# Kernel optimization log

Hardware: AMD Instinct MI355X
Metric: run time of the kernel (lower is better)

Reference implementation:

```python
import jax, jax.numpy as jnp
import numpy as np

B, A, S, T, DE, D3 = 8, 32, 16, 750, 25, 58
L, DZ = 4, 512
KL_P = 0.0002


def setup_inputs() -> dict:
    key = jax.random.key(0)
    ks = jax.random.split(key, 6)
    return {
        "gt_emotion": jax.random.normal(ks[0], (B * A, T, DE), jnp.float32),
        "gt_3dmm": jax.random.normal(ks[1], (B * A, T, D3), jnp.float32),
        "pred_emotion": jax.random.normal(ks[2], (B * S, T, DE), jnp.float32),
        "pred_3dmm": jax.random.normal(ks[3], (B * S, T, D3), jnp.float32),
        "dist_mu": jax.random.normal(ks[4], (L, B * S, DZ), jnp.float32),
        "dist_scale": jax.random.uniform(ks[5], (L, B * S, DZ), jnp.float32, 0.5, 1.5),
        "num_appropriate": jnp.full((B,), A, jnp.int32),
        "num_samples": jnp.full((B,), S, jnp.int32),
    }


def reference(gt_emotion, gt_3dmm, pred_emotion, pred_3dmm, dist_mu, dist_scale,
              num_appropriate, num_samples):
    b = num_appropriate.shape[0]
    a = gt_emotion.shape[0] // b      # appropriate reactions per batch element
    s = pred_emotion.shape[0] // b    # predicted samples per batch element
    t, de = gt_emotion.shape[1], gt_emotion.shape[2]
    d3 = gt_3dmm.shape[2]

    ge = gt_emotion.reshape(b, a, t, de)
    g3 = gt_3dmm.reshape(b, a, t, d3)
    pe = pred_emotion.reshape(b, s, t, de)
    p3 = pred_3dmm.reshape(b, s, t, d3)

    # pairwise mean-MSE cost between every pred sample and every appropriate gt
    ce = jnp.mean((pe[:, :, None] - ge[:, None]) ** 2, axis=(3, 4))                    # [b,s,a]
    c1 = jnp.mean((p3[:, :, None, :, :52] - g3[:, None, :, :, :52]) ** 2, axis=(3, 4))
    c2 = jnp.mean((p3[:, :, None, :, 52:] - g3[:, None, :, :, 52:]) ** 2, axis=(3, 4))
    cost = ce + c1 + 10.0 * c2

    idx = jnp.argmin(cost, axis=2)                     # [b,s] best-match index (torch.no_grad)
    bidx = jnp.arange(b)[:, None]
    ge_sel = ge[bidx, idx]                             # [b,s,t,de] gathered gt
    g3_sel = g3[bidx, idx]                             # [b,s,t,d3]

    rec_loss = (jnp.mean((pe - ge_sel) ** 2)
                + jnp.mean((p3[..., :52] - g3_sel[..., :52]) ** 2)
                + 10.0 * jnp.mean((p3[..., 52:] - g3_sel[..., 52:]) ** 2))

    # KL(N(mu, scale) || N(0, 1)), mean per layer then averaged over layers
    kl = -jnp.log(dist_scale) + 0.5 * (dist_scale ** 2 + dist_mu ** 2 - 1.0)
    kld_loss = jnp.mean(kl)

    loss = rec_loss + KL_P * kld_loss
    return (loss, rec_loss, kld_loss)
```

## Files before the change

kernel.cpp:

```cpp
#include <hip/hip_runtime.h>

#define NB 8
#define NA 32
#define NS 16
#define KE 18750
#define K3 43500
#define KH_E 9375
#define KH_3 21750
#define ND3 58
#define NKL 262144

#define SE_SLABS 10
#define SD_SLABS 22
#define SLABS 32
#define CHE 938
#define CHD 989
#define COST_BLOCKS (NB * 8 * SLABS)
#define KL_BLOCKS 64
#define KL_PER_THR (NKL / (KL_BLOCKS * 256))

#define SW_1 0.0050637127f
#define SW_2 0.0471404521f
#define W_E  (1.0f / 18750.0f)

__global__ __launch_bounds__(256, 3) void fused_kernel(
    const float* __restrict__ ge, const float* __restrict__ g3,
    const float* __restrict__ pe, const float* __restrict__ p3,
    const float* __restrict__ mu, const float* __restrict__ sc,
    float* __restrict__ cost, float* __restrict__ klsum)
{
    const int blk = blockIdx.x;
    const int tid = threadIdx.x;
    __shared__ float red[4][64];

    if (blk < KL_BLOCKS) {
        float ks = 0.f;
        #pragma unroll
        for (int it = 0; it < KL_PER_THR; ++it) {
            const int i = blk * (256 * KL_PER_THR) + it * 256 + tid;
            const float m = mu[i], sg = sc[i];
            ks += 0.5f * (sg * sg + m * m - 1.0f) - logf(sg);
        }
        #pragma unroll
        for (int o = 32; o > 0; o >>= 1) ks += __shfl_xor(ks, o);
        const int lane = tid & 63, w = tid >> 6;
        if (lane == 0) red[0][w] = ks;
        __syncthreads();
        if (tid == 0)
            atomicAdd(klsum, red[0][0] + red[0][1] + red[0][2] + red[0][3]);
        return;
    }

    const int cblk = blk - KL_BLOCKS;
    const int b    = cblk >> 8;
    const int rem  = cblk & 255;
    const int pos  = rem >> 5;
    const int slab = rem & 31;
    const int s0   = (pos >> 2) * 8;
    const int a0   = (pos & 3) * 8;

    const bool isE = slab < SE_SLABS;

    float acc[64];
    #pragma unroll
    for (int i = 0; i < 64; ++i) acc[i] = 0.f;

    if (isE) {
        const int base = slab * CHE;
        const int kend = min(base + CHE, KH_E);
        const float2* __restrict__ P = (const float2*)(pe + (size_t)(b * NS + s0) * KE);
        const float2* __restrict__ G = (const float2*)(ge + (size_t)(b * NA + a0) * KE);

        int kk = base + tid;
        float2 p[8], g[8];
        #pragma unroll
        for (int i = 0; i < 8; ++i) p[i] = P[i * KH_E + kk];
        #pragma unroll
        for (int j = 0; j < 8; ++j) g[j] = G[j * KH_E + kk];

        #pragma unroll 1
        while (kk < kend) {
            const int knext = kk + 256;
            const int kload = (knext < kend) ? knext : kk;
            float2 pn[8], gn[8];
            #pragma unroll
            for (int i = 0; i < 8; ++i) pn[i] = P[i * KH_E + kload];
            #pragma unroll
            for (int j = 0; j < 8; ++j) gn[j] = G[j * KH_E + kload];

            #pragma unroll
            for (int i = 0; i < 8; ++i)
                #pragma unroll
                for (int j = 0; j < 8; ++j) {
                    const float d0 = p[i].x - g[j].x;
                    const float d1 = p[i].y - g[j].y;
                    float t = fmaf(d0, d0, acc[i * 8 + j]);
                    acc[i * 8 + j] = fmaf(d1, d1, t);
                }

            #pragma unroll
            for (int i = 0; i < 8; ++i) { p[i] = pn[i]; g[i] = gn[i]; }
            kk = knext;
        }
    } else {
        const int base = (slab - SE_SLABS) * CHD;
        const int kend = min(base + CHD, KH_3);
        const float2* __restrict__ P = (const float2*)(p3 + (size_t)(b * NS + s0) * K3);
        const float2* __restrict__ G = (const float2*)(g3 + (size_t)(b * NA + a0) * K3);

        int kk = base + tid;
        int col = (2 * kk) % ND3;
        float2 p[8], g[8];
        #pragma unroll
        for (int i = 0; i < 8; ++i) p[i] = P[i * KH_3 + kk];
        #pragma unroll
        for (int j = 0; j < 8; ++j) g[j] = G[j * KH_3 + kk];

        #pragma unroll 1
        while (kk < kend) {
            const int knext = kk + 256;
            const int kload = (knext < kend) ? knext : kk;
            float2 pn[8], gn[8];
            #pragma unroll
            for (int i = 0; i < 8; ++i) pn[i] = P[i * KH_3 + kload];
            #pragma unroll
            for (int j = 0; j < 8; ++j) gn[j] = G[j * KH_3 + kload];

            const float sw = (col < 52) ? SW_1 : SW_2;
            col += 48; if (col >= ND3) col -= ND3;

            float2 ps[8], gs[8];
            #pragma unroll
            for (int i = 0; i < 8; ++i) { ps[i].x = p[i].x * sw; ps[i].y = p[i].y * sw; }
            #pragma unroll
            for (int j = 0; j < 8; ++j) { gs[j].x = g[j].x * sw; gs[j].y = g[j].y * sw; }

            #pragma unroll
            for (int i = 0; i < 8; ++i)
                #pragma unroll
                for (int j = 0; j < 8; ++j) {
                    const float d0 = ps[i].x - gs[j].x;
                    const float d1 = ps[i].y - gs[j].y;
                    float t = fmaf(d0, d0, acc[i * 8 + j]);
                    acc[i * 8 + j] = fmaf(d1, d1, t);
                }

            #pragma unroll
            for (int i = 0; i < 8; ++i) { p[i] = pn[i]; g[i] = gn[i]; }
            kk = knext;
        }
    }

    const int lane = tid & 63;
    int n = 64;
    #pragma unroll
    for (int step = 0; step < 6; ++step) {
        const int o = 1 << step;
        const bool hi = (lane & o) != 0;
        const int h = n >> 1;
        #pragma unroll
        for (int m = 0; m < h; ++m) {
            const float send = hi ? acc[m] : acc[m + h];
            const float recv = __shfl_xor(send, o);
            acc[m] = (hi ? acc[m + h] : acc[m]) + recv;
        }
        n = h;
    }

    const int w = tid >> 6;
    red[w][__brev((unsigned)lane) >> 26] = acc[0];
    __syncthreads();
    if (tid < 64) {
        float v = red[0][tid] + red[1][tid] + red[2][tid] + red[3][tid];
        if (isE) v *= W_E;
        const int i = tid >> 3, j = tid & 7;
        atomicAdd(&cost[b * (NS * NA) + (s0 + i) * NA + (a0 + j)], v);
    }
}

__global__ __launch_bounds__(128) void finalize_kernel(
    const float* __restrict__ cost, const float* __restrict__ klsum,
    float* __restrict__ out)
{
    const int t = threadIdx.x;
    const float4* row = (const float4*)(cost + t * NA);
    float mn = 1e30f;
    #pragma unroll
    for (int q = 0; q < 8; ++q) {
        const float4 v = row[q];
        mn = fminf(mn, fminf(fminf(v.x, v.y), fminf(v.z, v.w)));
    }
    #pragma unroll
    for (int o = 32; o > 0; o >>= 1) mn += __shfl_xor(mn, o);
    __shared__ float r2[2];
    if ((t & 63) == 0) r2[t >> 6] = mn;
    __syncthreads();
    if (t == 0) {
        const float rec = (r2[0] + r2[1]) * (1.0f / (NB * NS));
        const float kld = klsum[0] * (1.0f / (float)NKL);
        out[0] = fmaf(0.0002f, kld, rec);
        out[1] = rec;
        out[2] = kld;
    }
}

extern "C" void kernel_launch(void* const* d_in, const int* in_sizes, int n_in,
                              void* d_out, int out_size, void* d_ws, size_t ws_size,
                              hipStream_t stream)
{
    const float* ge = (const float*)d_in[0];
    const float* g3 = (const float*)d_in[1];
    const float* pe = (const float*)d_in[2];
    const float* p3 = (const float*)d_in[3];
    const float* mu = (const float*)d_in[4];
    const float* sc = (const float*)d_in[5];

    float* cost  = (float*)d_ws;
    float* klsum = cost + NB * NS * NA;

    hipMemsetAsync(d_ws, 0, (NB * NS * NA + 1) * sizeof(float), stream);

    fused_kernel<<<COST_BLOCKS + KL_BLOCKS, 256, 0, stream>>>(
        ge, g3, pe, p3, mu, sc, cost, klsum);
    finalize_kernel<<<1, 128, 0, stream>>>(cost, klsum, (float*)d_out);
}
```

Before: 146.0 us.

## Stage pairwise-cost operands through LDS with async global_load_lds double buffering

Replaces direct per-thread float2 register prefetch with asynchronous global-to-LDS loads (global_load_lds, 16 bytes per lane) into a per-wave double buffer, synchronised with explicit vmcnt waits. The reduction dimension is re-split into fixed 256-float2 chunks across fewer, larger slabs (12 per tile instead of 32), and the last partial chunk is masked with a weight. The aim is wider memory transactions, fewer in-flight registers and fewer redundant atomics and blocks. The cost is more LDS per block, occupancy lowered to 2, and reliance on hand-written waitcnt correctness.

```diff
diff --git a/kernel.cpp b/kernel.cpp
--- a/kernel.cpp
+++ b/kernel.cpp
@@ -1,4 +1,5 @@
 #include <hip/hip_runtime.h>
+#include <stdint.h>
 
 #define NB 8
 #define NA 32
@@ -10,11 +11,12 @@
 #define ND3 58
 #define NKL 262144
 
-#define SE_SLABS 10
-#define SD_SLABS 22
-#define SLABS 32
-#define CHE 938
-#define CHD 989
+#define CHUNK_F2 256
+#define NCH_E 37
+#define NCH_D 85
+#define E_SLABS 4
+#define D_SLABS 8
+#define SLABS 12
 #define COST_BLOCKS (NB * 8 * SLABS)
 #define KL_BLOCKS 64
 #define KL_PER_THR (NKL / (KL_BLOCKS * 256))
@@ -23,15 +25,19 @@
 #define SW_2 0.0471404521f
 #define W_E  (1.0f / 18750.0f)
 
-__global__ __launch_bounds__(256, 3) void fused_kernel(
+__global__ __launch_bounds__(256, 2) void fused_kernel(
     const float* __restrict__ ge, const float* __restrict__ g3,
     const float* __restrict__ pe, const float* __restrict__ p3,
     const float* __restrict__ mu, const float* __restrict__ sc,
     float* __restrict__ cost, float* __restrict__ klsum)
 {
+    __shared__ float lds[4][2][16][128];
+    float* red = &lds[0][0][0][0];
+
     const int blk = blockIdx.x;
     const int tid = threadIdx.x;
-    __shared__ float red[4][64];
+    const int w   = tid >> 6;
+    const int l   = tid & 63;
 
     if (blk < KL_BLOCKS) {
         float ks = 0.f;
@@ -43,51 +49,75 @@
         }
         #pragma unroll
         for (int o = 32; o > 0; o >>= 1) ks += __shfl_xor(ks, o);
-        const int lane = tid & 63, w = tid >> 6;
-        if (lane == 0) red[0][w] = ks;
+        if (l == 0) red[w] = ks;
         __syncthreads();
         if (tid == 0)
-            atomicAdd(klsum, red[0][0] + red[0][1] + red[0][2] + red[0][3]);
+            atomicAdd(klsum, red[0] + red[1] + red[2] + red[3]);
         return;
     }
 
     const int cblk = blk - KL_BLOCKS;
-    const int b    = cblk >> 8;
-    const int rem  = cblk & 255;
-    const int pos  = rem >> 5;
-    const int slab = rem & 31;
+    const int b    = cblk / (8 * SLABS);
+    const int rem  = cblk % (8 * SLABS);
+    const int pos  = rem / SLABS;
+    const int slab = rem % SLABS;
     const int s0   = (pos >> 2) * 8;
     const int a0   = (pos & 3) * 8;
 
-    const bool isE = slab < SE_SLABS;
+    const bool isE = slab < E_SLABS;
+    const int  KF  = isE ? KE : K3;
+    const int  KH  = isE ? KH_E : KH_3;
+    int clo, chi;
+    if (isE) { clo = slab * NCH_E / E_SLABS; chi = (slab + 1) * NCH_E / E_SLABS; }
+    else {
+        const int ds = slab - E_SLABS;
+        clo = ds * NCH_D / D_SLABS; chi = (ds + 1) * NCH_D / D_SLABS;
+    }
+
+    const float* __restrict__ Pr = isE ? pe + (size_t)(b * NS + s0) * KE
+                                       : p3 + (size_t)(b * NS + s0) * K3;
+    const float* __restrict__ Gr = isE ? ge + (size_t)(b * NA + a0) * KE
+                                       : g3 + (size_t)(b * NA + a0) * K3;
+
+    float* wb0 = &lds[w][0][0][0];
+    float* wb1 = &lds[w][1][0][0];
 
     float acc[64];
     #pragma unroll
     for (int i = 0; i < 64; ++i) acc[i] = 0.f;
 
+    const int rsel = l >> 5;
+    const int coff = (l & 31) * 2;
+    auto STAGE = [&](int c, float* wb) {
+        int f2 = c * CHUNK_F2 + w * 64 + coff;
+        f2 = (f2 <= KH - 2) ? f2 : (KH - 2);
+        #pragma unroll
+        for (int t = 0; t < 8; ++t) {
+            const float* src = (t < 4)
+                ? Pr + (size_t)(2 * t + rsel) * KF + 2 * f2
+                : Gr + (size_t)(2 * (t - 4) + rsel) * KF + 2 * f2;
+            __builtin_amdgcn_global_load_lds(
+                (const __attribute__((address_space(1))) uint32_t*)src,
+                (__attribute__((address_space(3))) uint32_t*)(wb + t * 256),
+                16, 0, 0);
+        }
+    };
+
+    int col = (2 * (clo * CHUNK_F2 + w * 64 + l)) % ND3;
+
+    STAGE(clo, (clo & 1) ? wb1 : wb0);
+
     if (isE) {
-        const int base = slab * CHE;
-        const int kend = min(base + CHE, KH_E);
-        const float2* __restrict__ P = (const float2*)(pe + (size_t)(b * NS + s0) * KE);
-        const float2* __restrict__ G = (const float2*)(ge + (size_t)(b * NA + a0) * KE);
-
-        int kk = base + tid;
-        float2 p[8], g[8];
-        #pragma unroll
-        for (int i = 0; i < 8; ++i) p[i] = P[i * KH_E + kk];
-        #pragma unroll
-        for (int j = 0; j < 8; ++j) g[j] = G[j * KH_E + kk];
-
         #pragma unroll 1
-        while (kk < kend) {
-            const int knext = kk + 256;
-            const int kload = (knext < kend) ? knext : kk;
-            float2 pn[8], gn[8];
-            #pragma unroll
-            for (int i = 0; i < 8; ++i) pn[i] = P[i * KH_E + kload];
-            #pragma unroll
-            for (int j = 0; j < 8; ++j) gn[j] = G[j * KH_E + kload];
-
+        for (int c = clo; c < chi - 1; ++c) {
+            STAGE(c + 1, ((c + 1) & 1) ? wb1 : wb0);
+            asm volatile("s_waitcnt vmcnt(8)" ::: "memory");
+            const float* wb = (c & 1) ? wb1 : wb0;
+            float2 p[8], g[8];
+            #pragma unroll
+            for (int i = 0; i < 8; ++i) p[i] = *(const float2*)(wb + i * 128 + 2 * l);
+            #pragma unroll
+            for (int j = 0; j < 8; ++j) g[j] = *(const float2*)(wb + (8 + j) * 128 + 2 * l);
             #pragma unroll
             for (int i = 0; i < 8; ++i)
                 #pragma unroll
@@ -97,66 +127,69 @@
                     float t = fmaf(d0, d0, acc[i * 8 + j]);
                     acc[i * 8 + j] = fmaf(d1, d1, t);
                 }
-
-            #pragma unroll
-            for (int i = 0; i < 8; ++i) { p[i] = pn[i]; g[i] = gn[i]; }
-            kk = knext;
         }
     } else {
-        const int base = (slab - SE_SLABS) * CHD;
-        const int kend = min(base + CHD, KH_3);
-        const float2* __restrict__ P = (const float2*)(p3 + (size_t)(b * NS + s0) * K3);
-        const float2* __restrict__ G = (const float2*)(g3 + (size_t)(b * NA + a0) * K3);
-
-        int kk = base + tid;
-        int col = (2 * kk) % ND3;
-        float2 p[8], g[8];
-        #pragma unroll
-        for (int i = 0; i < 8; ++i) p[i] = P[i * KH_3 + kk];
-        #pragma unroll
-        for (int j = 0; j < 8; ++j) g[j] = G[j * KH_3 + kk];
-
         #pragma unroll 1
-        while (kk < kend) {
-            const int knext = kk + 256;
-            const int kload = (knext < kend) ? knext : kk;
-            float2 pn[8], gn[8];
-            #pragma unroll
-            for (int i = 0; i < 8; ++i) pn[i] = P[i * KH_3 + kload];
-            #pragma unroll
-            for (int j = 0; j < 8; ++j) gn[j] = G[j * KH_3 + kload];
-
+        for (int c = clo; c < chi - 1; ++c) {
+            STAGE(c + 1, ((c + 1) & 1) ? wb1 : wb0);
+            asm volatile("s_waitcnt vmcnt(8)" ::: "memory");
+            const float* wb = (c & 1) ? wb1 : wb0;
             const float sw = (col < 52) ? SW_1 : SW_2;
             col += 48; if (col >= ND3) col -= ND3;
-
-            float2 ps[8], gs[8];
-            #pragma unroll
-            for (int i = 0; i < 8; ++i) { ps[i].x = p[i].x * sw; ps[i].y = p[i].y * sw; }
-            #pragma unroll
-            for (int j = 0; j < 8; ++j) { gs[j].x = g[j].x * sw; gs[j].y = g[j].y * sw; }
-
+            float2 p[8], g[8];
+            #pragma unroll
+            for (int i = 0; i < 8; ++i) p[i] = *(const float2*)(wb + i * 128 + 2 * l);
+            #pragma unroll
+            for (int j = 0; j < 8; ++j) g[j] = *(const float2*)(wb + (8 + j) * 128 + 2 * l);
+            #pragma unroll
+            for (int i = 0; i < 8; ++i) { p[i].x *= sw; p[i].y *= sw; }
+            #pragma unroll
+            for (int j = 0; j < 8; ++j) { g[j].x *= sw; g[j].y *= sw; }
             #pragma unroll
             for (int i = 0; i < 8; ++i)
                 #pragma unroll
                 for (int j = 0; j < 8; ++j) {
-                    const float d0 = ps[i].x - gs[j].x;
-                    const float d1 = ps[i].y - gs[j].y;
+                    const float d0 = p[i].x - g[j].x;
+                    const float d1 = p[i].y - g[j].y;
                     float t = fmaf(d0, d0, acc[i * 8 + j]);
                     acc[i * 8 + j] = fmaf(d1, d1, t);
                 }
-
-            #pragma unroll
-            for (int i = 0; i < 8; ++i) { p[i] = pn[i]; g[i] = gn[i]; }
-            kk = knext;
-        }
-    }
-
-    const int lane = tid & 63;
+        }
+    }
+
+    {
+        asm volatile("s_waitcnt vmcnt(0)" ::: "memory");
+        const int c = chi - 1;
+        const float* wb = (c & 1) ? wb1 : wb0;
+        const int fi = c * CHUNK_F2 + w * 64 + l;
+        float wl;
+        if (isE) wl = (fi < KH) ? 1.f : 0.f;
+        else     wl = (fi < KH) ? ((col < 52) ? SW_1 : SW_2) : 0.f;
+        float2 p[8], g[8];
+        #pragma unroll
+        for (int i = 0; i < 8; ++i) p[i] = *(const float2*)(wb + i * 128 + 2 * l);
+        #pragma unroll
+        for (int j = 0; j < 8; ++j) g[j] = *(const float2*)(wb + (8 + j) * 128 + 2 * l);
+        #pragma unroll
+        for (int i = 0; i < 8; ++i) { p[i].x *= wl; p[i].y *= wl; }
+        #pragma unroll
+        for (int j = 0; j < 8; ++j) { g[j].x *= wl; g[j].y *= wl; }
+        #pragma unroll
+        for (int i = 0; i < 8; ++i)
+            #pragma unroll
+            for (int j = 0; j < 8; ++j) {
+                const float d0 = p[i].x - g[j].x;
+                const float d1 = p[i].y - g[j].y;
+                float t = fmaf(d0, d0, acc[i * 8 + j]);
+                acc[i * 8 + j] = fmaf(d1, d1, t);
+            }
+    }
+
     int n = 64;
     #pragma unroll
     for (int step = 0; step < 6; ++step) {
         const int o = 1 << step;
-        const bool hi = (lane & o) != 0;
+        const bool hi = (l & o) != 0;
         const int h = n >> 1;
         #pragma unroll
         for (int m = 0; m < h; ++m) {
@@ -167,11 +200,12 @@
         n = h;
     }
 
-    const int w = tid >> 6;
-    red[w][__brev((unsigned)lane) >> 26] = acc[0];
+    __syncthreads();
+    red[w * 64 + (__brev((unsigned)l) >> 26)] = acc[0];
     __syncthreads();
     if (tid < 64) {
-        float v = red[0][tid] + red[1][tid] + red[2][tid] + red[3][tid];
+        float v = red[0 * 64 + tid] + red[1 * 64 + tid]
+                + red[2 * 64 + tid] + red[3 * 64 + tid];
         if (isE) v *= W_E;
         const int i = tid >> 3, j = tid & 7;
         atomicAdd(&cost[b * (NS * NA) + (s0 + i) * NA + (a0 + j)], v);
```

After: 147.4 us. No clear change (+1.0%).
